# Performance work log

Measured on AMD Instinct MI355X. Metric: run time of the kernel, lower is better.

## Reference

```python
import math
import jax, jax.numpy as jnp
import numpy as np

B, DIM, L = 2, 512, 2048
H = 16
HD = DIM // H  # 32
R = 32
K = 3
GAMMA = 1.0


def _conv1d(x, w, b=None):
    # x: [B, Cin, L], w: [Cout, Cin, K] -> [B, Cout, L_out] (VALID)
    out = jax.lax.conv_general_dilated(
        x, w, window_strides=(1,), padding='VALID',
        dimension_numbers=('NCH', 'OIH', 'NCH'))
    if b is not None:
        out = out + b[None, :, None]
    return out


def _sketch_p4(x, G1, G2):
    # x: [B, H, L, HD]; G1, G2: [HD, R]
    # p=4: half = (1/sqrt(r)) * (x@G1 * x@G2); return half*half
    half = (x @ G1) * (x @ G2) / math.sqrt(R)
    return half * half  # [B, H, L, R]


def setup_inputs() -> dict:
    key = jax.random.key(0)
    ks = jax.random.split(key, 12)
    x = jax.random.normal(ks[0], (B, DIM, L), dtype=jnp.float32)
    # conv / linear params (kaiming-ish scale)
    q_w = jax.random.normal(ks[1], (DIM, DIM, K), dtype=jnp.float32) / math.sqrt(DIM * K)
    q_b = jnp.zeros((DIM,), dtype=jnp.float32)
    k_w = jax.random.normal(ks[2], (DIM, DIM, K), dtype=jnp.float32) / math.sqrt(DIM * K)
    k_b = jnp.zeros((DIM,), dtype=jnp.float32)
    v_w = jax.random.normal(ks[3], (DIM, DIM, 1), dtype=jnp.float32) / math.sqrt(DIM)
    proj_w = jax.random.normal(ks[4], (DIM, DIM), dtype=jnp.float32) / math.sqrt(DIM)
    proj_b = jnp.zeros((DIM,), dtype=jnp.float32)
    # learnable scalars
    gamma_q = jnp.ones((1,), dtype=jnp.float32) * GAMMA
    beta_q = jnp.zeros((1,), dtype=jnp.float32)
    gamma_k = jnp.ones((1,), dtype=jnp.float32) * GAMMA
    beta_k = jnp.zeros((1,), dtype=jnp.float32)
    # sketch matrices, std = 1/sqrt(r)
    G1q = jax.random.normal(ks[5], (HD, R), dtype=jnp.float32) / math.sqrt(R)
    G2q = jax.random.normal(ks[6], (HD, R), dtype=jnp.float32) / math.sqrt(R)
    G1k = jax.random.normal(ks[7], (HD, R), dtype=jnp.float32) / math.sqrt(R)
    G2k = jax.random.normal(ks[8], (HD, R), dtype=jnp.float32) / math.sqrt(R)
    return dict(x=x, q_w=q_w, q_b=q_b, k_w=k_w, k_b=k_b, v_w=v_w,
                proj_w=proj_w, proj_b=proj_b,
                gamma_q=gamma_q, beta_q=beta_q, gamma_k=gamma_k, beta_k=beta_k,
                G1q=G1q, G2q=G2q, G1k=G1k, G2k=G2k)


def reference(x, q_w, q_b, k_w, k_b, v_w, proj_w, proj_b,
              gamma_q, beta_q, gamma_k, beta_k, G1q, G2q, G1k, G2k):
    batch, dim, length = x.shape
    # causal left pad by K-1
    x_pad = jnp.pad(x, ((0, 0), (0, 0), (K - 1, 0)))
    q = _conv1d(x_pad, q_w, q_b)   # [B, DIM, L]
    k = _conv1d(x_pad, k_w, k_b)   # [B, DIM, L]
    v = _conv1d(x, v_w)            # [B, DIM, L] (1x1 conv, no bias)

    def shape(t):
        # [B, DIM, L] -> [B, H, HD, L] -> [B, H, L, HD]
        return t.reshape(batch, H, HD, length).transpose(0, 1, 3, 2)

    q, k, v = shape(q), shape(k), shape(v)
    q = gamma_q * q + beta_q
    k = gamma_k * k + beta_k
    phi_q = _sketch_p4(q, G1q, G2q)  # [B, H, L, R]
    phi_k = _sketch_p4(k, G1k, G2k)  # [B, H, L, R]
    scores = jnp.einsum('bhlr,bhmr->bhlm', phi_q, phi_k)  # [B, H, L, L]
    attn = scores / (scores.sum(axis=-1, keepdims=True) + 1e-6)
    o = jnp.einsum('bhlm,bhmd->bhld', attn, v)  # [B, H, L, HD]
    # [B, H, L, HD] -> [B, H, HD, L] -> [B, DIM, L] -> [B, L, DIM]
    o = o.transpose(0, 1, 3, 2).reshape(batch, dim, length).transpose(0, 2, 1)
    return o @ proj_w.T + proj_b
```

## Files before the change

kernel.cpp:

```cpp
#include <hip/hip_runtime.h>
#include <hip/hip_bf16.h>

#define DIMC 512
#define LEN  2048
#define NH   16
#define HD   32
#define RR   32

typedef __bf16 bf8_t __attribute__((ext_vector_type(8)));
typedef __bf16 bf4_t __attribute__((ext_vector_type(4)));
typedef float  f4_t  __attribute__((ext_vector_type(4)));

__device__ __forceinline__ void gload16(const void* g, void* l) {
    __builtin_amdgcn_global_load_lds(
        (const __attribute__((address_space(1))) unsigned int*)g,
        (__attribute__((address_space(3))) unsigned int*)l, 16, 0, 0);
}

__device__ __forceinline__ int fswz(int col) {
    return (col ^ (col >> 2) ^ (col >> 4)) & 3;
}

__global__ __launch_bounds__(256) void prep_kernel(
    const float* __restrict__ x,
    const float* __restrict__ qw, const float* __restrict__ kw,
    const float* __restrict__ vw, const float* __restrict__ pw,
    const float* __restrict__ G1q, const float* __restrict__ G2q,
    const float* __restrict__ G1k, const float* __restrict__ G2k,
    __bf16* __restrict__ xTh, __bf16* __restrict__ xTl,
    __bf16* __restrict__ Wrh, __bf16* __restrict__ Wrl,
    __bf16* __restrict__ pwh, __bf16* __restrict__ pwl,
    __bf16* __restrict__ GTh, __bf16* __restrict__ GTl,
    float* __restrict__ Skv)
{
    const int bid = blockIdx.x;
    const int tid = threadIdx.x;
    if (bid < 512) {
        __shared__ float tile[64][65];
        const int lblk = bid & 31, cblk = (bid >> 5) & 7, b = bid >> 8;
        const int l0 = lblk * 64, c0 = cblk * 64;
        #pragma unroll
        for (int it = 0; it < 4; ++it) {
            int cl = (tid >> 4) + it * 16;
            int ll = (tid & 15) * 4;
            float4 v4 = *reinterpret_cast<const float4*>(
                x + ((size_t)b * DIMC + c0 + cl) * LEN + l0 + ll);
            tile[cl][ll+0] = v4.x; tile[cl][ll+1] = v4.y;
            tile[cl][ll+2] = v4.z; tile[cl][ll+3] = v4.w;
        }
        __syncthreads();
        const int l  = tid & 63;
        const int cs = (tid >> 6) * 16;
        size_t rowbase = ((size_t)b * 2050 + l0 + l + 2) * DIMC + c0;
        #pragma unroll
        for (int half = 0; half < 2; ++half) {
            int c = cs + half * 8;
            bf8_t hi, lo;
            #pragma unroll
            for (int e = 0; e < 8; ++e) {
                float f = tile[c + e][l];
                __bf16 h = (__bf16)f;
                hi[e] = h;
                lo[e] = (__bf16)(f - (float)h);
            }
            *reinterpret_cast<bf8_t*>(xTh + rowbase + c) = hi;
            *reinterpret_cast<bf8_t*>(xTl + rowbase + c) = lo;
        }
        if (lblk == 0 && cblk == 0) {
            size_t pb = (size_t)b * 2050 * DIMC;
            #pragma unroll
            for (int e = 0; e < 4; ++e) {
                int p = tid * 4 + e;
                xTh[pb + p] = (__bf16)0.f;
                xTl[pb + p] = (__bf16)0.f;
            }
        }
    } else if (bid < 2048) {
        __shared__ float raw[1536];
        const int m = bid - 512;
        const float* srow;
        int len;
        if (m < 512)       { srow = qw + (size_t)m * 1536;         len = 1536; }
        else if (m < 1024) { srow = kw + (size_t)(m - 512) * 1536; len = 1536; }
        else               { srow = vw + (size_t)(m - 1024) * 512; len = 512;  }
        for (int i = tid; i < len; i += 256) raw[i] = srow[i];
        __syncthreads();
        const bool isv = (m >= 1024);
        for (int c8 = tid; c8 < 192; c8 += 256) {
            int o   = c8 * 8;
            int kk  = o >> 9, ci0 = o & 511;
            bf8_t hi, lo;
            #pragma unroll
            for (int e = 0; e < 8; ++e) {
                float f;
                if (!isv) f = raw[(ci0 + e) * 3 + kk];
                else      f = (kk == 2) ? raw[ci0 + e] : 0.f;
                __bf16 h = (__bf16)f;
                hi[e] = h;
                lo[e] = (__bf16)(f - (float)h);
            }
            *reinterpret_cast<bf8_t*>(Wrh + (size_t)m * 1536 + o) = hi;
            *reinterpret_cast<bf8_t*>(Wrl + (size_t)m * 1536 + o) = lo;
        }
    } else if (bid < 2304) {
        int idx = (bid - 2048) * 1024 + tid * 4;
        float4 v4 = *reinterpret_cast<const float4*>(pw + idx);
        float vv[4] = {v4.x, v4.y, v4.z, v4.w};
        bf4_t hi, lo;
        #pragma unroll
        for (int e = 0; e < 4; ++e) {
            __bf16 h = (__bf16)vv[e];
            hi[e] = h;
            lo[e] = (__bf16)(vv[e] - (float)h);
        }
        *reinterpret_cast<bf4_t*>(pwh + idx) = hi;
        *reinterpret_cast<bf4_t*>(pwl + idx) = lo;
    } else if (bid < 2436) {
        int idx = (bid - 2304) * 256 + tid;
        Skv[idx] = 0.f;
    } else {
        #pragma unroll
        for (int m = 0; m < 4; ++m) {
            const float* g = (m == 0) ? G1q : (m == 1) ? G2q : (m == 2) ? G1k : G2k;
            #pragma unroll
            for (int e = 0; e < 4; ++e) {
                int i = tid * 4 + e;
                int r = i >> 5, d = i & 31;
                float f = g[d * 32 + r];
                __bf16 h = (__bf16)f;
                GTh[m * 1024 + i] = h;
                GTl[m * 1024 + i] = (__bf16)(f - (float)h);
            }
        }
    }
}

__global__ __launch_bounds__(256) void conv_mfma_kernel(
    const __bf16* __restrict__ xTh, const __bf16* __restrict__ xTl,
    const __bf16* __restrict__ Wrh, const __bf16* __restrict__ Wrl,
    const float* __restrict__ q_b, const float* __restrict__ k_b,
    float* __restrict__ q, float* __restrict__ k, float* __restrict__ v)
{
    __shared__ __bf16 sAh[128 * 32], sAl[128 * 32], sBh[64 * 32], sBl[64 * 32];
    const int b   = blockIdx.z;
    const int mg  = blockIdx.y * 128;
    const int n0  = blockIdx.x * 64;
    const int tid = threadIdx.x;
    const int wave = tid >> 6, lane = tid & 63;
    const int wm = wave >> 1, wn = wave & 1;
    const int lr = lane & 15, k8 = lane >> 4;
    const int sec = mg >> 9;
    const int kks = (sec == 2) ? 2 : 0;

    const __bf16* xh = xTh + (size_t)b * 2050 * DIMC;
    const __bf16* xl = xTl + (size_t)b * 2050 * DIMC;

    f4_t acc[4][2];
    #pragma unroll
    for (int i = 0; i < 4; ++i)
        #pragma unroll
        for (int j = 0; j < 2; ++j)
            #pragma unroll
            for (int e = 0; e < 4; ++e) acc[i][j][e] = 0.f;

    const int sr0 = tid >> 2;
    const int ss  = tid & 3;
    const int sk0 = ((ss ^ ((sr0 >> 1) & 3)) << 3);
    const int sr1 = sr0 + 64;
    const int sk1 = ((ss ^ ((sr1 >> 1) & 3)) << 3);

    for (int kk = kks; kk < 3; ++kk) {
        const __bf16* wAh = Wrh + (size_t)mg * 1536 + kk * 512;
        const __bf16* wAl = Wrl + (size_t)mg * 1536 + kk * 512;
        const __bf16* xbh = xh + (size_t)(n0 + kk) * DIMC;
        const __bf16* xbl = xl + (size_t)(n0 + kk) * DIMC;
        for (int k0 = 0; k0 < 512; k0 += 32) {
            gload16(wAh + (size_t)sr0 * 1536 + k0 + sk0, (char*)sAh + tid * 16);
            gload16(wAh + (size_t)sr1 * 1536 + k0 + sk1, (char*)sAh + (256 + tid) * 16);
            gload16(wAl + (size_t)sr0 * 1536 + k0 + sk0, (char*)sAl + tid * 16);
            gload16(wAl + (size_t)sr1 * 1536 + k0 + sk1, (char*)sAl + (256 + tid) * 16);
            gload16(xbh + (size_t)sr0 * DIMC + k0 + sk0, (char*)sBh + tid * 16);
            gload16(xbl + (size_t)sr0 * DIMC + k0 + sk0, (char*)sBl + tid * 16);
            __syncthreads();
            bf8_t ah[4], al[4], bh[2], bl[2];
            #pragma unroll
            for (int i = 0; i < 4; ++i) {
                int row = wm * 64 + i * 16 + lr;
                int off = row * 64 + ((k8 ^ ((row >> 1) & 3)) << 4);
                ah[i] = *(const bf8_t*)((const char*)sAh + off);
                al[i] = *(const bf8_t*)((const char*)sAl + off);
            }
            #pragma unroll
            for (int j = 0; j < 2; ++j) {
                int row = wn * 32 + j * 16 + lr;
                int off = row * 64 + ((k8 ^ ((row >> 1) & 3)) << 4);
                bh[j] = *(const bf8_t*)((const char*)sBh + off);
                bl[j] = *(const bf8_t*)((const char*)sBl + off);
            }
            #pragma unroll
            for (int i = 0; i < 4; ++i)
                #pragma unroll
                for (int j = 0; j < 2; ++j) {
                    acc[i][j] = __builtin_amdgcn_mfma_f32_16x16x32_bf16(ah[i], bh[j], acc[i][j], 0, 0, 0);
                    acc[i][j] = __builtin_amdgcn_mfma_f32_16x16x32_bf16(ah[i], bl[j], acc[i][j], 0, 0, 0);
                    acc[i][j] = __builtin_amdgcn_mfma_f32_16x16x32_bf16(al[i], bh[j], acc[i][j], 0, 0, 0);
                }
            __syncthreads();
        }
    }
    float* outp = (sec == 0) ? q : (sec == 1) ? k : v;
    const float* bp = (sec == 0) ? q_b : (sec == 1) ? k_b : nullptr;
    const int cob = mg & 511;
    #pragma unroll
    for (int i = 0; i < 4; ++i)
        #pragma unroll
        for (int r = 0; r < 4; ++r) {
            int co = cob + wm * 64 + i * 16 + k8 * 4 + r;
            float bv = bp ? bp[co] : 0.f;
            float* orow = outp + ((size_t)b * DIMC + co) * LEN;
            #pragma unroll
            for (int j = 0; j < 2; ++j)
                orow[n0 + wn * 32 + j * 16 + lr] = acc[i][j][r] + bv;
        }
}

__global__ __launch_bounds__(256) void sketch_fused_kernel(
    const float* __restrict__ q, const float* __restrict__ k,
    const float* __restrict__ v,
    const float* __restrict__ gamma_q, const float* __restrict__ beta_q,
    const float* __restrict__ gamma_k, const float* __restrict__ beta_k,
    const __bf16* __restrict__ GTh, const __bf16* __restrict__ GTl,
    float* __restrict__ phi_q, float* __restrict__ Skv, float* __restrict__ sk)
{
    __shared__ __align__(16) char smem[17424];
    __bf16* sBh = (__bf16*)smem;
    __bf16* sBl = (__bf16*)(smem + 8192);
    const int z = blockIdx.z;
    const int b = z & 1, isk = z >> 1;
    const int h0 = blockIdx.y * 2;
    const int l0 = blockIdx.x * 64;
    const int tid = threadIdx.x;
    const int wave = tid >> 6, lane = tid & 63;
    const int lr = lane & 15, k8 = lane >> 4;

    const float* src = isk ? k : q;
    const float ga = isk ? gamma_k[0] : gamma_q[0];
    const float be = isk ? beta_k[0]  : beta_q[0];

    #pragma unroll
    for (int it = 0; it < 4; ++it) {
        int f = it * 256 + tid;
        int row = f >> 4;
        int l4  = (f & 15) * 4;
        float4 v4 = *reinterpret_cast<const float4*>(
            src + ((size_t)b * DIMC + h0 * 32 + row) * LEN + l0 + l4);
        int d = row & 31, hloc = row >> 5;
        float vv[4] = {v4.x, v4.y, v4.z, v4.w};
        #pragma unroll
        for (int e = 0; e < 4; ++e) {
            float qp = ga * vv[e] + be;
            __bf16 hh = (__bf16)qp;
            int col = hloc * 64 + l4 + e;
            int off = col * 32 + (((d >> 3) ^ fswz(col)) << 3) + (d & 7);
            sBh[off] = hh;
            sBl[off] = (__bf16)(qp - (float)hh);
        }
    }
    __syncthreads();

    const int cw = wave * 32;
    bf8_t bh[2], bl[2];
    #pragma unroll
    for (int nt = 0; nt < 2; ++nt) {
        int col = cw + nt * 16 + lr;
        int off = col * 32 + ((k8 ^ fswz(col)) << 3);
        bh[nt] = *(const bf8_t*)(sBh + off);
        bl[nt] = *(const bf8_t*)(sBl + off);
    }

    const int matb = isk * 2;
    f4_t t1[2][2], t2[2][2];
    #pragma unroll
    for (int mt = 0; mt < 2; ++mt)
        #pragma unroll
        for (int nt = 0; nt < 2; ++nt)
            #pragma unroll
            for (int e = 0; e < 4; ++e) { t1[mt][nt][e] = 0.f; t2[mt][nt][e] = 0.f; }

    #pragma unroll
    for (int mt = 0; mt < 2; ++mt) {
        int abase = matb * 1024 + (mt * 16 + lr) * 32 + k8 * 8;
        bf8_t a1h = *(const bf8_t*)(GTh + abase);
        bf8_t a1l = *(const bf8_t*)(GTl + abase);
        bf8_t a2h = *(const bf8_t*)(GTh + abase + 1024);
        bf8_t a2l = *(const bf8_t*)(GTl + abase + 1024);
        #pragma unroll
        for (int nt = 0; nt < 2; ++nt) {
            t1[mt][nt] = __builtin_amdgcn_mfma_f32_16x16x32_bf16(a1h, bh[nt], t1[mt][nt], 0, 0, 0);
            t1[mt][nt] = __builtin_amdgcn_mfma_f32_16x16x32_bf16(a1h, bl[nt], t1[mt][nt], 0, 0, 0);
            t1[mt][nt] = __builtin_amdgcn_mfma_f32_16x16x32_bf16(a1l, bh[nt], t1[mt][nt], 0, 0, 0);
            t2[mt][nt] = __builtin_amdgcn_mfma_f32_16x16x32_bf16(a2h, bh[nt], t2[mt][nt], 0, 0, 0);
            t2[mt][nt] = __builtin_amdgcn_mfma_f32_16x16x32_bf16(a2h, bl[nt], t2[mt][nt], 0, 0, 0);
            t2[mt][nt] = __builtin_amdgcn_mfma_f32_16x16x32_bf16(a2l, bh[nt], t2[mt][nt], 0, 0, 0);
        }
    }

    if (!isk) {
        #pragma unroll
        for (int mt = 0; mt < 2; ++mt)
            #pragma unroll
            for (int nt = 0; nt < 2; ++nt) {
                int col = cw + nt * 16 + lr;
                int l = col & 63, hloc = col >> 6;
                f4_t out;
                #pragma unroll
                for (int e = 0; e < 4; ++e) {
                    float hh = t1[mt][nt][e] * t2[mt][nt][e] * 0.17677669529663687f;
                    out[e] = hh * hh;
                }
                *reinterpret_cast<f4_t*>(phi_q +
                    (((size_t)b * NH + h0 + hloc) * LEN + l0 + l) * RR + mt * 16 + k8 * 4) = out;
            }
        return;
    }

    float* phiS = (float*)smem;
    float* vS   = (float*)(smem + 8448);
    const int r  = tid >> 3;
    const int d4 = (tid & 7) * 4;
    const int hl = wave >> 1;
    #pragma unroll
    for (int hph = 0; hph < 2; ++hph) {
        __syncthreads();
        if (hl == hph) {
            #pragma unroll
            for (int mt = 0; mt < 2; ++mt)
                #pragma unroll
                for (int nt = 0; nt < 2; ++nt) {
                    int l = (cw + nt * 16 + lr) & 63;
                    #pragma unroll
                    for (int e = 0; e < 4; ++e) {
                        float hh = t1[mt][nt][e] * t2[mt][nt][e] * 0.17677669529663687f;
                        phiS[l * 33 + mt * 16 + k8 * 4 + e] = hh * hh;
                    }
                }
        }
        const float* vb = v + ((size_t)b * DIMC + (h0 + hph) * HD) * LEN + l0;
        for (int i = tid; i < 64 * 32; i += 256) {
            int dd = i >> 6, lc = i & 63;
            vS[lc * 33 + dd] = vb[(size_t)dd * LEN + lc];
        }
        __syncthreads();
        float acc4[4] = {0.f, 0.f, 0.f, 0.f};
        float skacc = 0.f;
        #pragma unroll 8
        for (int lc = 0; lc < 64; ++lc) {
            float pv = phiS[lc * 33 + r];
            skacc += pv;
            #pragma unroll
            for (int j = 0; j < 4; ++j) acc4[j] += pv * vS[lc * 33 + d4 + j];
        }
        const size_t base = (size_t)(b * NH + h0 + hph) * RR + r;
        float* Sp = Skv + base * HD + d4;
        #pragma unroll
        for (int j = 0; j < 4; ++j) atomicAdd(Sp + j, acc4[j]);
        if ((tid & 7) == 0) atomicAdd(sk + base, skacc);
    }
}

__global__ __launch_bounds__(256) void onorm_kernel(
    const float* __restrict__ phi_q, const float* __restrict__ Skv,
    const float* __restrict__ sk, __bf16* __restrict__ o_h, __bf16* __restrict__ o_l)
{
    __shared__ float Ss[4][RR][HD];
    __shared__ float sks[4][RR];
    __shared__ float ph[32][RR + 1];
    const int b = blockIdx.z, hg = blockIdx.y;
    const int l0 = blockIdx.x * 32;
    const int tid = threadIdx.x;
    const int bh0 = b * NH + hg * 4;
    for (int i = tid; i < 4096; i += 256) {
        int hh = i >> 10;
        Ss[hh][(i >> 5) & 31][i & 31] = Skv[(size_t)(bh0 + hh) * (RR * HD) + (i & 1023)];
    }
    if (tid < 128) sks[tid >> 5][tid & 31] = sk[(size_t)(bh0 + (tid >> 5)) * RR + (tid & 31)];
    const int d = tid & 31, ls = tid >> 5;
    for (int h = 0; h < 4; ++h) {
        __syncthreads();
        for (int i = tid; i < 1024; i += 256)
            ph[i >> 5][i & 31] = phi_q[((size_t)(bh0 + h) * LEN + l0 + (i >> 5)) * RR + (i & 31)];
        __syncthreads();
        #pragma unroll
        for (int lt = 0; lt < 4; ++lt) {
            int l = lt * 8 + ls;
            float num = 0.f, den = 0.f;
            #pragma unroll
            for (int r = 0; r < RR; ++r) {
                float p = ph[l][r];
                num += p * Ss[h][r][d];
                den += p * sks[h][r];
            }
            float val = num / (den + 1e-6f);
            __bf16 hv = (__bf16)val;
            size_t oi = ((size_t)b * LEN + l0 + l) * DIMC + (hg * 4 + h) * HD + d;
            o_h[oi] = hv;
            o_l[oi] = (__bf16)(val - (float)hv);
        }
    }
}

__global__ __launch_bounds__(256) void proj_mfma_kernel(
    const __bf16* __restrict__ oh, const __bf16* __restrict__ ol,
    const __bf16* __restrict__ pwh, const __bf16* __restrict__ pwl,
    const float* __restrict__ pb, float* __restrict__ out)
{
    __shared__ __bf16 sAh[64 * 32], sAl[64 * 32], sBh[64 * 32], sBl[64 * 32];
    const int m0  = blockIdx.y * 64;
    const int n0  = blockIdx.x * 64;
    const int tid = threadIdx.x;
    const int wave = tid >> 6, lane = tid & 63;
    const int wm = wave >> 1, wn = wave & 1;
    const int lr = lane & 15, k8 = lane >> 4;

    f4_t acc[2][2];
    #pragma unroll
    for (int i = 0; i < 2; ++i)
        #pragma unroll
        for (int j = 0; j < 2; ++j)
            #pragma unroll
            for (int e = 0; e < 4; ++e) acc[i][j][e] = 0.f;

    const int sr0 = tid >> 2;
    const int ss  = tid & 3;
    const int sk0 = ((ss ^ ((sr0 >> 1) & 3)) << 3);

    for (int k0 = 0; k0 < 512; k0 += 32) {
        gload16(oh  + (size_t)(m0 + sr0) * DIMC + k0 + sk0, (char*)sAh + tid * 16);
        gload16(ol  + (size_t)(m0 + sr0) * DIMC + k0 + sk0, (char*)sAl + tid * 16);
        gload16(pwh + (size_t)(n0 + sr0) * DIMC + k0 + sk0, (char*)sBh + tid * 16);
        gload16(pwl + (size_t)(n0 + sr0) * DIMC + k0 + sk0, (char*)sBl + tid * 16);
        __syncthreads();
        bf8_t ah[2], al[2], bh[2], bl[2];
        #pragma unroll
        for (int i = 0; i < 2; ++i) {
            int row = wm * 32 + i * 16 + lr;
            int off = row * 64 + ((k8 ^ ((row >> 1) & 3)) << 4);
            ah[i] = *(const bf8_t*)((const char*)sAh + off);
            al[i] = *(const bf8_t*)((const char*)sAl + off);
        }
        #pragma unroll
        for (int j = 0; j < 2; ++j) {
            int row = wn * 32 + j * 16 + lr;
            int off = row * 64 + ((k8 ^ ((row >> 1) & 3)) << 4);
            bh[j] = *(const bf8_t*)((const char*)sBh + off);
            bl[j] = *(const bf8_t*)((const char*)sBl + off);
        }
        #pragma unroll
        for (int i = 0; i < 2; ++i)
            #pragma unroll
            for (int j = 0; j < 2; ++j) {
                acc[i][j] = __builtin_amdgcn_mfma_f32_16x16x32_bf16(ah[i], bh[j], acc[i][j], 0, 0, 0);
                acc[i][j] = __builtin_amdgcn_mfma_f32_16x16x32_bf16(ah[i], bl[j], acc[i][j], 0, 0, 0);
                acc[i][j] = __builtin_amdgcn_mfma_f32_16x16x32_bf16(al[i], bh[j], acc[i][j], 0, 0, 0);
            }
        __syncthreads();
    }
    #pragma unroll
    for (int j = 0; j < 2; ++j) {
        int n = n0 + wn * 32 + j * 16 + lr;
        float bv = pb[n];
        #pragma unroll
        for (int i = 0; i < 2; ++i)
            #pragma unroll
            for (int r = 0; r < 4; ++r) {
                int m = m0 + wm * 32 + i * 16 + k8 * 4 + r;
                out[(size_t)m * DIMC + n] = acc[i][j][r] + bv;
            }
    }
}

extern "C" void kernel_launch(void* const* d_in, const int* in_sizes, int n_in,
                              void* d_out, int out_size, void* d_ws, size_t ws_size,
                              hipStream_t stream)
{
    const float* x       = (const float*)d_in[0];
    const float* q_w     = (const float*)d_in[1];
    const float* q_b     = (const float*)d_in[2];
    const float* k_w     = (const float*)d_in[3];
    const float* k_b     = (const float*)d_in[4];
    const float* v_w     = (const float*)d_in[5];
    const float* proj_w  = (const float*)d_in[6];
    const float* proj_b  = (const float*)d_in[7];
    const float* gamma_q = (const float*)d_in[8];
    const float* beta_q  = (const float*)d_in[9];
    const float* gamma_k = (const float*)d_in[10];
    const float* beta_k  = (const float*)d_in[11];
    const float* G1q     = (const float*)d_in[12];
    const float* G2q     = (const float*)d_in[13];
    const float* G1k     = (const float*)d_in[14];
    const float* G2k     = (const float*)d_in[15];

    char* W = (char*)d_ws;
    constexpr size_t QKV  = (size_t)2 * DIMC * LEN * 4;
    constexpr size_t XT   = (size_t)2 * 2050 * DIMC * 2;
    constexpr size_t WR   = (size_t)1536 * 1536 * 2;
    constexpr size_t PW   = (size_t)DIMC * DIMC * 2;
    constexpr size_t GT   = (size_t)4 * 1024 * 2;

    float*  q    = (float*)(W);
    float*  k    = (float*)(W + QKV);
    float*  v    = (float*)(W + 2 * QKV);
    __bf16* xTh  = (__bf16*)(W + 3 * QKV);
    __bf16* xTl  = (__bf16*)(W + 3 * QKV + XT);
    __bf16* Wrh  = (__bf16*)(W + 3 * QKV + 2 * XT);
    __bf16* Wrl  = (__bf16*)(W + 3 * QKV + 2 * XT + WR);
    __bf16* pwh  = (__bf16*)(W + 3 * QKV + 2 * XT + 2 * WR);
    __bf16* pwl  = (__bf16*)(W + 3 * QKV + 2 * XT + 2 * WR + PW);
    __bf16* GTh  = (__bf16*)(W + 3 * QKV + 2 * XT + 2 * WR + 2 * PW);
    __bf16* GTl  = (__bf16*)(W + 3 * QKV + 2 * XT + 2 * WR + 2 * PW + GT);
    float*  Skv  = (float*)(W + 3 * QKV + 2 * XT + 2 * WR + 2 * PW + 2 * GT);
    float*  sk   = Skv + (size_t)2 * NH * RR * HD;
    float*  phi_q = (float*)xTh;
    __bf16* o_h   = (__bf16*)q;
    __bf16* o_l   = (__bf16*)(W + QKV / 2);

    prep_kernel<<<2437, 256, 0, stream>>>(x, q_w, k_w, v_w, proj_w,
                                          G1q, G2q, G1k, G2k,
                                          xTh, xTl, Wrh, Wrl, pwh, pwl,
                                          GTh, GTl, Skv);

    conv_mfma_kernel<<<dim3(LEN / 64, 12, 2), 256, 0, stream>>>(
        xTh, xTl, Wrh, Wrl, q_b, k_b, q, k, v);

    sketch_fused_kernel<<<dim3(LEN / 64, NH / 2, 4), 256, 0, stream>>>(
        q, k, v, gamma_q, beta_q, gamma_k, beta_k, GTh, GTl, phi_q, Skv, sk);

    onorm_kernel<<<dim3(LEN / 32, NH / 4, 2), 256, 0, stream>>>(
        phi_q, Skv, sk, o_h, o_l);

    proj_mfma_kernel<<<dim3(DIMC / 64, (2 * LEN) / 64), 256, 0, stream>>>(
        o_h, o_l, pwh, pwl, proj_b, (float*)d_out);
}
```

Before: 226.9 us.

## Fuse QKV conv GEMM with sketch and KV-state accumulation epilogue

Merges the conv MFMA kernel and the sketch kernel into one, so q/k/v are never written to or read back from global memory. Each block computes a 128-channel q or k tile; k blocks also compute the matching v tile into a second accumulator set. The sketch MFMAs, phi_q stores and Skv/sk atomics run as an epilogue from shared memory. The grid shrinks from 12 to 8 channel groups, which gives fewer blocks, longer k-blocks, and more accumulator registers that can lower occupancy. It also changes the prep transpose write pattern so each thread writes contiguous 16-byte row chunks.

```diff
diff --git a/kernel.cpp b/kernel.cpp
--- a/kernel.cpp
+++ b/kernel.cpp
@@ -49,22 +49,22 @@
             tile[cl][ll+2] = v4.z; tile[cl][ll+3] = v4.w;
         }
         __syncthreads();
-        const int l  = tid & 63;
-        const int cs = (tid >> 6) * 16;
-        size_t rowbase = ((size_t)b * 2050 + l0 + l + 2) * DIMC + c0;
+        const int t8 = tid & 7;
+        const int rr = tid >> 3;
         #pragma unroll
         for (int half = 0; half < 2; ++half) {
-            int c = cs + half * 8;
+            int row = rr + 32 * half;
+            size_t go = ((size_t)b * 2050 + l0 + row + 2) * DIMC + c0 + t8 * 8;
             bf8_t hi, lo;
             #pragma unroll
             for (int e = 0; e < 8; ++e) {
-                float f = tile[c + e][l];
+                float f = tile[t8 * 8 + e][row];
                 __bf16 h = (__bf16)f;
                 hi[e] = h;
                 lo[e] = (__bf16)(f - (float)h);
             }
-            *reinterpret_cast<bf8_t*>(xTh + rowbase + c) = hi;
-            *reinterpret_cast<bf8_t*>(xTl + rowbase + c) = lo;
+            *reinterpret_cast<bf8_t*>(xTh + go) = hi;
+            *reinterpret_cast<bf8_t*>(xTl + go) = lo;
         }
         if (lblk == 0 && cblk == 0) {
             size_t pb = (size_t)b * 2050 * DIMC;
@@ -135,33 +135,82 @@
     }
 }
 
-__global__ __launch_bounds__(256) void conv_mfma_kernel(
+#define KLOOP(AROWS, KKOFF, ACC)                                               \
+    {                                                                          \
+        const __bf16* wAh = Wrh + (size_t)(AROWS) * 1536 + (KKOFF) * 512;      \
+        const __bf16* wAl = Wrl + (size_t)(AROWS) * 1536 + (KKOFF) * 512;      \
+        const __bf16* xbh = xh + (size_t)(n0 + (KKOFF)) * DIMC;                \
+        const __bf16* xbl = xl + (size_t)(n0 + (KKOFF)) * DIMC;                \
+        for (int k0 = 0; k0 < 512; k0 += 32) {                                 \
+            gload16(wAh + (size_t)sr0 * 1536 + k0 + sk0, (char*)sAh + tid * 16);        \
+            gload16(wAh + (size_t)sr1 * 1536 + k0 + sk1, (char*)sAh + (256 + tid) * 16);\
+            gload16(wAl + (size_t)sr0 * 1536 + k0 + sk0, (char*)sAl + tid * 16);        \
+            gload16(wAl + (size_t)sr1 * 1536 + k0 + sk1, (char*)sAl + (256 + tid) * 16);\
+            gload16(xbh + (size_t)sr0 * DIMC + k0 + sk0, (char*)sBh + tid * 16);        \
+            gload16(xbl + (size_t)sr0 * DIMC + k0 + sk0, (char*)sBl + tid * 16);        \
+            __syncthreads();                                                   \
+            bf8_t ah[4], al[4], bh[2], bl[2];                                  \
+            _Pragma("unroll")                                                  \
+            for (int i = 0; i < 4; ++i) {                                      \
+                int row = wm * 64 + i * 16 + lr;                               \
+                int off = row * 64 + ((k8 ^ ((row >> 1) & 3)) << 4);           \
+                ah[i] = *(const bf8_t*)((const char*)sAh + off);               \
+                al[i] = *(const bf8_t*)((const char*)sAl + off);               \
+            }                                                                  \
+            _Pragma("unroll")                                                  \
+            for (int j = 0; j < 2; ++j) {                                      \
+                int row = wn * 32 + j * 16 + lr;                               \
+                int off = row * 64 + ((k8 ^ ((row >> 1) & 3)) << 4);           \
+                bh[j] = *(const bf8_t*)((const char*)sBh + off);               \
+                bl[j] = *(const bf8_t*)((const char*)sBl + off);               \
+            }                                                                  \
+            _Pragma("unroll")                                                  \
+            for (int i = 0; i < 4; ++i)                                        \
+                _Pragma("unroll")                                              \
+                for (int j = 0; j < 2; ++j) {                                  \
+                    ACC[i][j] = __builtin_amdgcn_mfma_f32_16x16x32_bf16(ah[i], bh[j], ACC[i][j], 0, 0, 0); \
+                    ACC[i][j] = __builtin_amdgcn_mfma_f32_16x16x32_bf16(ah[i], bl[j], ACC[i][j], 0, 0, 0); \
+                    ACC[i][j] = __builtin_amdgcn_mfma_f32_16x16x32_bf16(al[i], bh[j], ACC[i][j], 0, 0, 0); \
+                }                                                              \
+            __syncthreads();                                                   \
+        }                                                                      \
+    }
+
+__global__ __launch_bounds__(256) void fused_qkv_kernel(
     const __bf16* __restrict__ xTh, const __bf16* __restrict__ xTl,
     const __bf16* __restrict__ Wrh, const __bf16* __restrict__ Wrl,
     const float* __restrict__ q_b, const float* __restrict__ k_b,
-    float* __restrict__ q, float* __restrict__ k, float* __restrict__ v)
+    const float* __restrict__ gamma_q, const float* __restrict__ beta_q,
+    const float* __restrict__ gamma_k, const float* __restrict__ beta_k,
+    const __bf16* __restrict__ GTh, const __bf16* __restrict__ GTl,
+    float* __restrict__ phi_q, float* __restrict__ Skv, float* __restrict__ sk)
 {
-    __shared__ __bf16 sAh[128 * 32], sAl[128 * 32], sBh[64 * 32], sBl[64 * 32];
+    __shared__ __align__(16) char smem[24576];
+    __bf16* sAh = (__bf16*)smem;
+    __bf16* sAl = (__bf16*)(smem + 8192);
+    __bf16* sBh = (__bf16*)(smem + 16384);
+    __bf16* sBl = (__bf16*)(smem + 20480);
+
     const int b   = blockIdx.z;
-    const int mg  = blockIdx.y * 128;
+    const int ys  = blockIdx.y;
+    const int isk = ys >> 2;
+    const int cob = (ys & 3) * 128;
     const int n0  = blockIdx.x * 64;
     const int tid = threadIdx.x;
     const int wave = tid >> 6, lane = tid & 63;
     const int wm = wave >> 1, wn = wave & 1;
     const int lr = lane & 15, k8 = lane >> 4;
-    const int sec = mg >> 9;
-    const int kks = (sec == 2) ? 2 : 0;
 
     const __bf16* xh = xTh + (size_t)b * 2050 * DIMC;
     const __bf16* xl = xTl + (size_t)b * 2050 * DIMC;
 
-    f4_t acc[4][2];
+    f4_t acc[4][2], accv[4][2];
     #pragma unroll
     for (int i = 0; i < 4; ++i)
         #pragma unroll
         for (int j = 0; j < 2; ++j)
             #pragma unroll
-            for (int e = 0; e < 4; ++e) acc[i][j][e] = 0.f;
+            for (int e = 0; e < 4; ++e) { acc[i][j][e] = 0.f; accv[i][j][e] = 0.f; }
 
     const int sr0 = tid >> 2;
     const int ss  = tid & 3;
@@ -169,202 +218,144 @@
     const int sr1 = sr0 + 64;
     const int sk1 = ((ss ^ ((sr1 >> 1) & 3)) << 3);
 
-    for (int kk = kks; kk < 3; ++kk) {
-        const __bf16* wAh = Wrh + (size_t)mg * 1536 + kk * 512;
-        const __bf16* wAl = Wrl + (size_t)mg * 1536 + kk * 512;
-        const __bf16* xbh = xh + (size_t)(n0 + kk) * DIMC;
-        const __bf16* xbl = xl + (size_t)(n0 + kk) * DIMC;
-        for (int k0 = 0; k0 < 512; k0 += 32) {
-            gload16(wAh + (size_t)sr0 * 1536 + k0 + sk0, (char*)sAh + tid * 16);
-            gload16(wAh + (size_t)sr1 * 1536 + k0 + sk1, (char*)sAh + (256 + tid) * 16);
-            gload16(wAl + (size_t)sr0 * 1536 + k0 + sk0, (char*)sAl + tid * 16);
-            gload16(wAl + (size_t)sr1 * 1536 + k0 + sk1, (char*)sAl + (256 + tid) * 16);
-            gload16(xbh + (size_t)sr0 * DIMC + k0 + sk0, (char*)sBh + tid * 16);
-            gload16(xbl + (size_t)sr0 * DIMC + k0 + sk0, (char*)sBl + tid * 16);
-            __syncthreads();
-            bf8_t ah[4], al[4], bh[2], bl[2];
-            #pragma unroll
-            for (int i = 0; i < 4; ++i) {
-                int row = wm * 64 + i * 16 + lr;
-                int off = row * 64 + ((k8 ^ ((row >> 1) & 3)) << 4);
-                ah[i] = *(const bf8_t*)((const char*)sAh + off);
-                al[i] = *(const bf8_t*)((const char*)sAl + off);
-            }
-            #pragma unroll
-            for (int j = 0; j < 2; ++j) {
-                int row = wn * 32 + j * 16 + lr;
-                int off = row * 64 + ((k8 ^ ((row >> 1) & 3)) << 4);
-                bh[j] = *(const bf8_t*)((const char*)sBh + off);
-                bl[j] = *(const bf8_t*)((const char*)sBl + off);
-            }
-            #pragma unroll
-            for (int i = 0; i < 4; ++i)
-                #pragma unroll
-                for (int j = 0; j < 2; ++j) {
-                    acc[i][j] = __builtin_amdgcn_mfma_f32_16x16x32_bf16(ah[i], bh[j], acc[i][j], 0, 0, 0);
-                    acc[i][j] = __builtin_amdgcn_mfma_f32_16x16x32_bf16(ah[i], bl[j], acc[i][j], 0, 0, 0);
-                    acc[i][j] = __builtin_amdgcn_mfma_f32_16x16x32_bf16(al[i], bh[j], acc[i][j], 0, 0, 0);
-                }
-            __syncthreads();
-        }
-    }
-    float* outp = (sec == 0) ? q : (sec == 1) ? k : v;
-    const float* bp = (sec == 0) ? q_b : (sec == 1) ? k_b : nullptr;
-    const int cob = mg & 511;
-    #pragma unroll
-    for (int i = 0; i < 4; ++i)
-        #pragma unroll
-        for (int r = 0; r < 4; ++r) {
-            int co = cob + wm * 64 + i * 16 + k8 * 4 + r;
-            float bv = bp ? bp[co] : 0.f;
-            float* orow = outp + ((size_t)b * DIMC + co) * LEN;
-            #pragma unroll
-            for (int j = 0; j < 2; ++j)
-                orow[n0 + wn * 32 + j * 16 + lr] = acc[i][j][r] + bv;
-        }
-}
-
-__global__ __launch_bounds__(256) void sketch_fused_kernel(
-    const float* __restrict__ q, const float* __restrict__ k,
-    const float* __restrict__ v,
-    const float* __restrict__ gamma_q, const float* __restrict__ beta_q,
-    const float* __restrict__ gamma_k, const float* __restrict__ beta_k,
-    const __bf16* __restrict__ GTh, const __bf16* __restrict__ GTl,
-    float* __restrict__ phi_q, float* __restrict__ Skv, float* __restrict__ sk)
-{
-    __shared__ __align__(16) char smem[17424];
-    __bf16* sBh = (__bf16*)smem;
-    __bf16* sBl = (__bf16*)(smem + 8192);
-    const int z = blockIdx.z;
-    const int b = z & 1, isk = z >> 1;
-    const int h0 = blockIdx.y * 2;
-    const int l0 = blockIdx.x * 64;
-    const int tid = threadIdx.x;
-    const int wave = tid >> 6, lane = tid & 63;
-    const int lr = lane & 15, k8 = lane >> 4;
-
-    const float* src = isk ? k : q;
+    const int mg = isk * 512 + cob;
+    for (int kk = 0; kk < 3; ++kk) KLOOP(mg, kk, acc);
+    if (isk) KLOOP(1024 + cob, 2, accv);
+
     const float ga = isk ? gamma_k[0] : gamma_q[0];
     const float be = isk ? beta_k[0]  : beta_q[0];
-
-    #pragma unroll
-    for (int it = 0; it < 4; ++it) {
-        int f = it * 256 + tid;
-        int row = f >> 4;
-        int l4  = (f & 15) * 4;
-        float4 v4 = *reinterpret_cast<const float4*>(
-            src + ((size_t)b * DIMC + h0 * 32 + row) * LEN + l0 + l4);
-        int d = row & 31, hloc = row >> 5;
-        float vv[4] = {v4.x, v4.y, v4.z, v4.w};
-        #pragma unroll
-        for (int e = 0; e < 4; ++e) {
-            float qp = ga * vv[e] + be;
-            __bf16 hh = (__bf16)qp;
-            int col = hloc * 64 + l4 + e;
-            int off = col * 32 + (((d >> 3) ^ fswz(col)) << 3) + (d & 7);
-            sBh[off] = hh;
-            sBl[off] = (__bf16)(qp - (float)hh);
-        }
-    }
-    __syncthreads();
-
-    const int cw = wave * 32;
-    bf8_t bh[2], bl[2];
-    #pragma unroll
-    for (int nt = 0; nt < 2; ++nt) {
-        int col = cw + nt * 16 + lr;
-        int off = col * 32 + ((k8 ^ fswz(col)) << 3);
-        bh[nt] = *(const bf8_t*)(sBh + off);
-        bl[nt] = *(const bf8_t*)(sBl + off);
-    }
-
+    const float* bp = isk ? k_b : q_b;
+    const int h0 = cob >> 5;
     const int matb = isk * 2;
-    f4_t t1[2][2], t2[2][2];
-    #pragma unroll
-    for (int mt = 0; mt < 2; ++mt)
-        #pragma unroll
-        for (int nt = 0; nt < 2; ++nt)
-            #pragma unroll
-            for (int e = 0; e < 4; ++e) { t1[mt][nt][e] = 0.f; t2[mt][nt][e] = 0.f; }
-
-    #pragma unroll
-    for (int mt = 0; mt < 2; ++mt) {
-        int abase = matb * 1024 + (mt * 16 + lr) * 32 + k8 * 8;
-        bf8_t a1h = *(const bf8_t*)(GTh + abase);
-        bf8_t a1l = *(const bf8_t*)(GTl + abase);
-        bf8_t a2h = *(const bf8_t*)(GTh + abase + 1024);
-        bf8_t a2l = *(const bf8_t*)(GTl + abase + 1024);
-        #pragma unroll
-        for (int nt = 0; nt < 2; ++nt) {
-            t1[mt][nt] = __builtin_amdgcn_mfma_f32_16x16x32_bf16(a1h, bh[nt], t1[mt][nt], 0, 0, 0);
-            t1[mt][nt] = __builtin_amdgcn_mfma_f32_16x16x32_bf16(a1h, bl[nt], t1[mt][nt], 0, 0, 0);
-            t1[mt][nt] = __builtin_amdgcn_mfma_f32_16x16x32_bf16(a1l, bh[nt], t1[mt][nt], 0, 0, 0);
-            t2[mt][nt] = __builtin_amdgcn_mfma_f32_16x16x32_bf16(a2h, bh[nt], t2[mt][nt], 0, 0, 0);
-            t2[mt][nt] = __builtin_amdgcn_mfma_f32_16x16x32_bf16(a2h, bl[nt], t2[mt][nt], 0, 0, 0);
-            t2[mt][nt] = __builtin_amdgcn_mfma_f32_16x16x32_bf16(a2l, bh[nt], t2[mt][nt], 0, 0, 0);
-        }
-    }
-
-    if (!isk) {
-        #pragma unroll
-        for (int mt = 0; mt < 2; ++mt)
-            #pragma unroll
-            for (int nt = 0; nt < 2; ++nt) {
-                int col = cw + nt * 16 + lr;
-                int l = col & 63, hloc = col >> 6;
-                f4_t out;
-                #pragma unroll
-                for (int e = 0; e < 4; ++e) {
-                    float hh = t1[mt][nt][e] * t2[mt][nt][e] * 0.17677669529663687f;
-                    out[e] = hh * hh;
-                }
-                *reinterpret_cast<f4_t*>(phi_q +
-                    (((size_t)b * NH + h0 + hloc) * LEN + l0 + l) * RR + mt * 16 + k8 * 4) = out;
-            }
-        return;
-    }
-
+    __bf16* skh = (__bf16*)smem;
+    __bf16* skl = (__bf16*)(smem + 8192);
     float* phiS = (float*)smem;
     float* vS   = (float*)(smem + 8448);
-    const int r  = tid >> 3;
-    const int d4 = (tid & 7) * 4;
-    const int hl = wave >> 1;
+
     #pragma unroll
-    for (int hph = 0; hph < 2; ++hph) {
-        __syncthreads();
-        if (hl == hph) {
+    for (int p = 0; p < 2; ++p) {
+        __syncthreads();
+        if (wm == p) {
+            #pragma unroll
+            for (int i = 0; i < 4; ++i) {
+                const int hloc = i >> 1;
+                #pragma unroll
+                for (int r = 0; r < 4; ++r) {
+                    int cl = i * 16 + k8 * 4 + r;
+                    int d  = cl & 31;
+                    float bv = bp[cob + p * 64 + cl];
+                    #pragma unroll
+                    for (int j = 0; j < 2; ++j) {
+                        float qp = ga * (acc[i][j][r] + bv) + be;
+                        __bf16 hh = (__bf16)qp;
+                        int col = hloc * 64 + wn * 32 + j * 16 + lr;
+                        int off = col * 32 + (((d >> 3) ^ fswz(col)) << 3) + (d & 7);
+                        skh[off] = hh;
+                        skl[off] = (__bf16)(qp - (float)hh);
+                    }
+                }
+            }
+        }
+        __syncthreads();
+        const int cw = wave * 32;
+        bf8_t bhf[2], blf[2];
+        #pragma unroll
+        for (int nt = 0; nt < 2; ++nt) {
+            int col = cw + nt * 16 + lr;
+            int off = col * 32 + ((k8 ^ fswz(col)) << 3);
+            bhf[nt] = *(const bf8_t*)(skh + off);
+            blf[nt] = *(const bf8_t*)(skl + off);
+        }
+        f4_t t1[2][2], t2[2][2];
+        #pragma unroll
+        for (int mt = 0; mt < 2; ++mt)
+            #pragma unroll
+            for (int nt = 0; nt < 2; ++nt)
+                #pragma unroll
+                for (int e = 0; e < 4; ++e) { t1[mt][nt][e] = 0.f; t2[mt][nt][e] = 0.f; }
+        #pragma unroll
+        for (int mt = 0; mt < 2; ++mt) {
+            int abase = matb * 1024 + (mt * 16 + lr) * 32 + k8 * 8;
+            bf8_t a1h = *(const bf8_t*)(GTh + abase);
+            bf8_t a1l = *(const bf8_t*)(GTl + abase);
+            bf8_t a2h = *(const bf8_t*)(GTh + abase + 1024);
+            bf8_t a2l = *(const bf8_t*)(GTl + abase + 1024);
+            #pragma unroll
+            for (int nt = 0; nt < 2; ++nt) {
+                t1[mt][nt] = __builtin_amdgcn_mfma_f32_16x16x32_bf16(a1h, bhf[nt], t1[mt][nt], 0, 0, 0);
+                t1[mt][nt] = __builtin_amdgcn_mfma_f32_16x16x32_bf16(a1h, blf[nt], t1[mt][nt], 0, 0, 0);
+                t1[mt][nt] = __builtin_amdgcn_mfma_f32_16x16x32_bf16(a1l, bhf[nt], t1[mt][nt], 0, 0, 0);
+                t2[mt][nt] = __builtin_amdgcn_mfma_f32_16x16x32_bf16(a2h, bhf[nt], t2[mt][nt], 0, 0, 0);
+                t2[mt][nt] = __builtin_amdgcn_mfma_f32_16x16x32_bf16(a2h, blf[nt], t2[mt][nt], 0, 0, 0);
+                t2[mt][nt] = __builtin_amdgcn_mfma_f32_16x16x32_bf16(a2l, bhf[nt], t2[mt][nt], 0, 0, 0);
+            }
+        }
+
+        if (!isk) {
             #pragma unroll
             for (int mt = 0; mt < 2; ++mt)
                 #pragma unroll
                 for (int nt = 0; nt < 2; ++nt) {
-                    int l = (cw + nt * 16 + lr) & 63;
+                    int col = cw + nt * 16 + lr;
+                    int l = col & 63, hloc = col >> 6;
+                    f4_t out;
                     #pragma unroll
                     for (int e = 0; e < 4; ++e) {
                         float hh = t1[mt][nt][e] * t2[mt][nt][e] * 0.17677669529663687f;
-                        phiS[l * 33 + mt * 16 + k8 * 4 + e] = hh * hh;
+                        out[e] = hh * hh;
                     }
+                    *reinterpret_cast<f4_t*>(phi_q +
+                        (((size_t)b * NH + h0 + 2 * p + hloc) * LEN + n0 + l) * RR + mt * 16 + k8 * 4) = out;
                 }
-        }
-        const float* vb = v + ((size_t)b * DIMC + (h0 + hph) * HD) * LEN + l0;
-        for (int i = tid; i < 64 * 32; i += 256) {
-            int dd = i >> 6, lc = i & 63;
-            vS[lc * 33 + dd] = vb[(size_t)dd * LEN + lc];
-        }
-        __syncthreads();
-        float acc4[4] = {0.f, 0.f, 0.f, 0.f};
-        float skacc = 0.f;
-        #pragma unroll 8
-        for (int lc = 0; lc < 64; ++lc) {
-            float pv = phiS[lc * 33 + r];
-            skacc += pv;
-            #pragma unroll
-            for (int j = 0; j < 4; ++j) acc4[j] += pv * vS[lc * 33 + d4 + j];
-        }
-        const size_t base = (size_t)(b * NH + h0 + hph) * RR + r;
-        float* Sp = Skv + base * HD + d4;
-        #pragma unroll
-        for (int j = 0; j < 4; ++j) atomicAdd(Sp + j, acc4[j]);
-        if ((tid & 7) == 0) atomicAdd(sk + base, skacc);
+        } else {
+            #pragma unroll
+            for (int hph = 0; hph < 2; ++hph) {
+                __syncthreads();
+                if (wm == hph) {
+                    #pragma unroll
+                    for (int mt = 0; mt < 2; ++mt)
+                        #pragma unroll
+                        for (int nt = 0; nt < 2; ++nt) {
+                            int col = cw + nt * 16 + lr;
+                            int l = col & 63;
+                            #pragma unroll
+                            for (int e = 0; e < 4; ++e) {
+                                float hh = t1[mt][nt][e] * t2[mt][nt][e] * 0.17677669529663687f;
+                                phiS[l * 33 + mt * 16 + k8 * 4 + e] = hh * hh;
+                            }
+                        }
+                }
+                if (wm == p) {
+                    #pragma unroll
+                    for (int ii = 0; ii < 2; ++ii)
+                        #pragma unroll
+                        for (int j = 0; j < 2; ++j)
+                            #pragma unroll
+                            for (int r = 0; r < 4; ++r) {
+                                int d = ii * 16 + k8 * 4 + r;
+                                int l = wn * 32 + j * 16 + lr;
+                                vS[l * 33 + d] = accv[2 * hph + ii][j][r];
+                            }
+                }
+                __syncthreads();
+                const int r2 = tid >> 3;
+                const int d4 = (tid & 7) * 4;
+                float a4[4] = {0.f, 0.f, 0.f, 0.f};
+                float ska = 0.f;
+                #pragma unroll 8
+                for (int lc = 0; lc < 64; ++lc) {
+                    float pv = phiS[lc * 33 + r2];
+                    ska += pv;
+                    #pragma unroll
+                    for (int j = 0; j < 4; ++j) a4[j] += pv * vS[lc * 33 + d4 + j];
+                }
+                const size_t base = (size_t)(b * NH + h0 + 2 * p + hph) * RR + r2;
+                float* Sp = Skv + base * HD + d4;
+                #pragma unroll
+                for (int j = 0; j < 4; ++j) atomicAdd(Sp + j, a4[j]);
+                if ((tid & 7) == 0) atomicAdd(sk + base, ska);
+            }
+        }
     }
 }
 
@@ -501,39 +492,35 @@
     const float* G2k     = (const float*)d_in[15];
 
     char* W = (char*)d_ws;
-    constexpr size_t QKV  = (size_t)2 * DIMC * LEN * 4;
     constexpr size_t XT   = (size_t)2 * 2050 * DIMC * 2;
     constexpr size_t WR   = (size_t)1536 * 1536 * 2;
     constexpr size_t PW   = (size_t)DIMC * DIMC * 2;
     constexpr size_t GT   = (size_t)4 * 1024 * 2;
-
-    float*  q    = (float*)(W);
-    float*  k    = (float*)(W + QKV);
-    float*  v    = (float*)(W + 2 * QKV);
-    __bf16* xTh  = (__bf16*)(W + 3 * QKV);
-    __bf16* xTl  = (__bf16*)(W + 3 * QKV + XT);
-    __bf16* Wrh  = (__bf16*)(W + 3 * QKV + 2 * XT);
-    __bf16* Wrl  = (__bf16*)(W + 3 * QKV + 2 * XT + WR);
-    __bf16* pwh  = (__bf16*)(W + 3 * QKV + 2 * XT + 2 * WR);
-    __bf16* pwl  = (__bf16*)(W + 3 * QKV + 2 * XT + 2 * WR + PW);
-    __bf16* GTh  = (__bf16*)(W + 3 * QKV + 2 * XT + 2 * WR + 2 * PW);
-    __bf16* GTl  = (__bf16*)(W + 3 * QKV + 2 * XT + 2 * WR + 2 * PW + GT);
-    float*  Skv  = (float*)(W + 3 * QKV + 2 * XT + 2 * WR + 2 * PW + 2 * GT);
+    constexpr size_t SKVB = (size_t)2 * NH * RR * HD * 4;
+    constexpr size_t SKB  = (size_t)2 * NH * RR * 4;
+
+    __bf16* xTh  = (__bf16*)(W);
+    __bf16* xTl  = (__bf16*)(W + XT);
+    __bf16* Wrh  = (__bf16*)(W + 2 * XT);
+    __bf16* Wrl  = (__bf16*)(W + 2 * XT + WR);
+    __bf16* pwh  = (__bf16*)(W + 2 * XT + 2 * WR);
+    __bf16* pwl  = (__bf16*)(W + 2 * XT + 2 * WR + PW);
+    __bf16* GTh  = (__bf16*)(W + 2 * XT + 2 * WR + 2 * PW);
+    __bf16* GTl  = (__bf16*)(W + 2 * XT + 2 * WR + 2 * PW + GT);
+    float*  Skv  = (float*)(W + 2 * XT + 2 * WR + 2 * PW + 2 * GT);
     float*  sk   = Skv + (size_t)2 * NH * RR * HD;
-    float*  phi_q = (float*)xTh;
-    __bf16* o_h   = (__bf16*)q;
-    __bf16* o_l   = (__bf16*)(W + QKV / 2);
+    float*  phi_q = (float*)(W + 2 * XT + 2 * WR + 2 * PW + 2 * GT + SKVB + SKB);
+    __bf16* o_h  = xTh;
+    __bf16* o_l  = xTl;
 
     prep_kernel<<<2437, 256, 0, stream>>>(x, q_w, k_w, v_w, proj_w,
                                           G1q, G2q, G1k, G2k,
                                           xTh, xTl, Wrh, Wrl, pwh, pwl,
                                           GTh, GTl, Skv);
 
-    conv_mfma_kernel<<<dim3(LEN / 64, 12, 2), 256, 0, stream>>>(
-        xTh, xTl, Wrh, Wrl, q_b, k_b, q, k, v);
-
-    sketch_fused_kernel<<<dim3(LEN / 64, NH / 2, 4), 256, 0, stream>>>(
-        q, k, v, gamma_q, beta_q, gamma_k, beta_k, GTh, GTl, phi_q, Skv, sk);
+    fused_qkv_kernel<<<dim3(LEN / 64, 8, 2), 256, 0, stream>>>(
+        xTh, xTl, Wrh, Wrl, q_b, k_b, gamma_q, beta_q, gamma_k, beta_k,
+        GTh, GTl, phi_q, Skv, sk);
 
     onorm_kernel<<<dim3(LEN / 32, NH / 4, 2), 256, 0, stream>>>(
         phi_q, Skv, sk, o_h, o_l);
```

After: 225.4 us. About the same (-0.7%).
